# Optimization experiments

Hardware: AMD Instinct MI355X
Metric: run time of the kernel (lower is better)

Reference implementation:

```python
import jax, jax.numpy as jnp
import numpy as np

N_NODES = 50000
N_EDGES = 500000
D = 128  # input_dim == output_dim -> residual is identity


def _linear(x, W, b):
    return x @ W + b


def setup_inputs() -> dict:
    rng = np.random.default_rng(0)
    ei = rng.integers(0, N_NODES, size=(2, N_EDGES))
    # one-time structure cache: unique (src,dst) pairs + multiplicity counts
    pairs = np.stack([ei[0], ei[1]], axis=1)
    uniq, counts = np.unique(pairs, axis=0, return_counts=True)

    key = jax.random.key(0)
    ks = jax.random.split(key, 16)
    s = 0.02
    inp = {
        "x": jax.random.normal(ks[0], (N_NODES, D), jnp.float32),
        "src": jnp.asarray(uniq[:, 0], jnp.int32),
        "dst": jnp.asarray(uniq[:, 1], jnp.int32),
        "counts": jnp.asarray(counts, jnp.float32),
        # lin_src_to_dst / lin_dst_to_src (stored as [in, out])
        "W_sd": jax.random.normal(ks[1], (D, D), jnp.float32) * s,
        "b_sd": jnp.zeros((D,), jnp.float32),
        "W_ds": jax.random.normal(ks[2], (D, D), jnp.float32) * s,
        "b_ds": jnp.zeros((D,), jnp.float32),
        # lcs_mlp: Linear(2D, D) -> ReLU -> Linear(D, 1)
        "W_l1": jax.random.normal(ks[3], (2 * D, D), jnp.float32) * s,
        "b_l1": jnp.zeros((D,), jnp.float32),
        "W_l2": jax.random.normal(ks[4], (D, 1), jnp.float32) * s,
        "b_l2": jnp.zeros((1,), jnp.float32),
        # gate_mlp: Linear(2D, D) -> ReLU -> Linear(D, 1)
        "W_g1": jax.random.normal(ks[5], (2 * D, D), jnp.float32) * s,
        "b_g1": jnp.zeros((D,), jnp.float32),
        "W_g2": jax.random.normal(ks[6], (D, 1), jnp.float32) * s,
        "b_g2": jnp.zeros((1,), jnp.float32),
    }
    return inp


def reference(x, src, dst, counts, W_sd, b_sd, W_ds, b_ds,
              W_l1, b_l1, W_l2, b_l2, W_g1, b_g1, W_g2, b_g2):
    num_nodes = x.shape[0]
    x_src = x[src]                      # [E, D] gather
    x_dst = x[dst]                      # [E, D] gather

    # LCS score per unique edge (computed under no_grad in torch -> stop_gradient)
    lcs_in = jnp.concatenate([x_src, x_dst], axis=-1)           # [E, 2D]
    h = jax.nn.relu(_linear(lcs_in, W_l1, b_l1))
    lcs = jax.nn.sigmoid(_linear(h, W_l2, b_l2))                # [E, 1]
    lcs = jax.lax.stop_gradient(lcs)

    cnt = counts[:, None]                                       # [E, 1]
    msg_in = _linear(x_src, W_sd, b_sd) * lcs * cnt             # [E, D]
    msg_out = _linear(x_dst, W_ds, b_ds) * lcs * cnt            # [E, D]

    h_in = jax.ops.segment_sum(msg_in, dst, num_segments=num_nodes)
    h_out = jax.ops.segment_sum(msg_out, src, num_segments=num_nodes)

    in_deg = jnp.clip(jax.ops.segment_sum(counts, dst, num_segments=num_nodes), 1.0)
    out_deg = jnp.clip(jax.ops.segment_sum(counts, src, num_segments=num_nodes), 1.0)
    h_in = h_in / in_deg[:, None]
    h_out = h_out / out_deg[:, None]

    gate_in = jnp.concatenate([h_in, h_out], axis=-1)           # [N, 2D]
    g = jax.nn.relu(_linear(gate_in, W_g1, b_g1))
    gate = jax.nn.sigmoid(_linear(g, W_g2, b_g2))               # [N, 1]

    fused = gate * h_in + (1.0 - gate) * h_out
    return fused + x  # residual is Identity (input_dim == output_dim)
```

## Files before the change

kernel.cpp:

```cpp
#include <hip/hip_runtime.h>
#include <math.h>

typedef unsigned int uint;
typedef unsigned long long ull;

#define THREADS 256
#define NC 96

typedef __attribute__((ext_vector_type(8))) short bf16x8;
typedef __attribute__((ext_vector_type(4))) float f32x4;

__device__ __forceinline__ float blo(uint u) { return __uint_as_float(u << 16); }
__device__ __forceinline__ float bhi(uint u) { return __uint_as_float(u & 0xffff0000u); }
__device__ __forceinline__ uint  bf16r(float x) {
    uint u = __float_as_uint(x);
    return (u + 0x7fffu + ((u >> 16) & 1u)) >> 16;
}
__device__ __forceinline__ uint packbf(float lo, float hi) {
    return bf16r(lo) | (bf16r(hi) << 16);
}

__global__ __launch_bounds__(THREADS)
void transpose_w(const float* __restrict__ W_sd, const float* __restrict__ W_ds,
                 const float* __restrict__ W_l1, const float* __restrict__ W_g1,
                 ushort* __restrict__ Wt, ushort* __restrict__ Wtg1)
{
    __shared__ float tile[32][33];
    const int y = blockIdx.y;
    const float* src;
    ushort* dst;
    int dstK, kofs;
    if (y < 4) {
        src = (y == 0) ? W_sd : (y == 1) ? W_ds : (y == 2) ? W_l1 : (W_l1 + 16384);
        dst = Wt + y * 16384; dstK = 128; kofs = 0;
    } else {
        src = W_g1 + (y - 4) * 16384;
        dst = Wtg1; dstK = 256; kofs = (y - 4) * 128;
    }
    const int tix = blockIdx.x;
    const int k0 = (tix & 3) * 32, n0 = (tix >> 2) * 32;
    const int t = threadIdx.x;

    {
        const int r = t >> 3, c8 = t & 7;
        const float4 f = *(const float4*)(src + (size_t)(k0 + r) * 128 + n0 + c8 * 4);
        tile[r][c8 * 4 + 0] = f.x; tile[r][c8 * 4 + 1] = f.y;
        tile[r][c8 * 4 + 2] = f.z; tile[r][c8 * 4 + 3] = f.w;
    }
    __syncthreads();
    {
        const int n = t >> 3, k8 = t & 7;
        const float v0 = tile[k8 * 4 + 0][n], v1 = tile[k8 * 4 + 1][n];
        const float v2 = tile[k8 * 4 + 2][n], v3 = tile[k8 * 4 + 3][n];
        uint2 o; o.x = packbf(v0, v1); o.y = packbf(v2, v3);
        *(uint2*)(dst + (size_t)(n0 + n) * dstK + kofs + k0 + k8 * 4) = o;
    }
}

__device__ __forceinline__ void mfma_tile_compute(const char* AsB, const char* BtB,
                                                  int wv, int ln, f32x4 acc[8])
{
    const int mrow = wv * 16 + (ln & 15);
    const int kgb  = (ln >> 4) * 16;
#pragma unroll
    for (int kk = 0; kk < 4; ++kk) {
        const int kbyte = kk * 64 + kgb;
        const bf16x8 a = *(const bf16x8*)(AsB + mrow * 256 + (kbyte ^ ((mrow & 7) << 4)));
#pragma unroll
        for (int tt = 0; tt < 8; ++tt) {
            const int nrow = tt * 16 + (ln & 15);
            const bf16x8 b = *(const bf16x8*)(BtB + nrow * 256 + (kbyte ^ ((nrow & 7) << 4)));
            acc[tt] = __builtin_amdgcn_mfma_f32_16x16x32_bf16(a, b, acc[tt], 0, 0, 0);
        }
    }
}

__global__ __launch_bounds__(THREADS)
void gemm_node_count(const float* __restrict__ X, int M,
                     const ushort* __restrict__ Wt,
                     const float* __restrict__ b_sd, const float* __restrict__ b_ds,
                     const float* __restrict__ b_l1,
                     ushort* __restrict__ Pb,
                     const int* __restrict__ src, const int* __restrict__ dst,
                     const float* __restrict__ counts,
                     ull* __restrict__ packed_in, int* __restrict__ off_out,
                     int E)
{
    __shared__ __align__(16) char AsB[16384];
    __shared__ __align__(16) char BtB[32768];

    const int tid = threadIdx.x;
    const int bid = blockIdx.x;

    if (bid < NC) {
        const int stride = NC * THREADS;
        for (int e = bid * THREADS + tid; e < E; e += stride) {
            const int  d = dst[e];
            const uint c = (uint)counts[e];
            atomicAdd(packed_in + d, (1ULL << 32) | (ull)c);
        }
        for (int e = bid * THREADS + tid; e < E; e += stride) {
            const int cur  = src[e];
            const int prev = (e == 0) ? -1 : src[e - 1];
            for (int v = prev + 1; v <= cur; ++v) off_out[v] = e;
            if (e == E - 1)
                for (int v = cur + 1; v <= M; ++v) off_out[v] = E;
        }
        return;
    }

    const int m0 = (bid - NC) * 64;
    const int wv = tid >> 6, ln = tid & 63;

    {
        const int r = tid >> 2, seg = tid & 3;
        int gr = m0 + r; if (gr >= M) gr = M - 1;
        const float4* xs = (const float4*)(X + (size_t)gr * 128 + seg * 32);
#pragma unroll
        for (int i = 0; i < 4; ++i) {
            const float4 f0 = xs[i * 2], f1 = xs[i * 2 + 1];
            uint4 u;
            u.x = packbf(f0.x, f0.y); u.y = packbf(f0.z, f0.w);
            u.z = packbf(f1.x, f1.y); u.w = packbf(f1.z, f1.w);
            const int kbyte = seg * 64 + i * 16;
            *(uint4*)(AsB + r * 256 + (kbyte ^ ((r & 7) << 4))) = u;
        }
    }

    for (int grp = 0; grp < 4; ++grp) {
        {
            const int rn = tid >> 1, sg = tid & 1;
            const uint4* ws = (const uint4*)(Wt + grp * 16384 + (size_t)rn * 128 + sg * 64);
#pragma unroll
            for (int i = 0; i < 8; ++i) {
                const uint4 u = ws[i];
                const int kbyte = sg * 128 + i * 16;
                *(uint4*)(BtB + rn * 256 + (kbyte ^ ((rn & 7) << 4))) = u;
            }
        }
        __syncthreads();

        f32x4 acc[8];
#pragma unroll
        for (int tt = 0; tt < 8; ++tt) acc[tt] = (f32x4){0.f, 0.f, 0.f, 0.f};
        mfma_tile_compute(AsB, BtB, wv, ln, acc);
        __syncthreads();

        const float* bias = (grp == 0) ? b_sd : (grp == 1) ? b_ds
                          : (grp == 2) ? b_l1 : nullptr;
#pragma unroll
        for (int tt = 0; tt < 8; ++tt) {
            const int n  = tt * 16 + (ln & 15);
            const float bv = bias ? bias[n] : 0.f;
#pragma unroll
            for (int r = 0; r < 4; ++r) {
                const int m = wv * 16 + ((ln >> 4) << 2) + r;
                ((ushort*)BtB)[m * 136 + n] = (ushort)bf16r(acc[tt][r] + bv);
            }
        }
        __syncthreads();
        {
            const int rr = tid >> 2, sg2 = tid & 3;
            const int gr = m0 + rr;
            if (gr < M) {
                uint4* dstp = (uint4*)Pb + (size_t)gr * 64 + grp * 16 + sg2 * 4;
#pragma unroll
                for (int i = 0; i < 4; ++i)
                    dstp[i] = *(const uint4*)(BtB + rr * 272 + (sg2 * 4 + i) * 16);
            }
        }
        __syncthreads();
    }
}

__global__ __launch_bounds__(256)
void scan_p1(const ull* __restrict__ packed_in, int* __restrict__ bsum, int M)
{
    __shared__ int s[256];
    const int t = threadIdx.x;
    const int i = blockIdx.x * 256 + t;
    s[t] = (i < M) ? (int)(packed_in[i] >> 32) : 0;
    __syncthreads();
#pragma unroll
    for (int o = 128; o; o >>= 1) {
        if (t < o) s[t] += s[t + o];
        __syncthreads();
    }
    if (t == 0) bsum[blockIdx.x] = s[0];
}

__global__ __launch_bounds__(1024)
void scan_p2(int* __restrict__ bsum, int NB)
{
    __shared__ int s[1024];
    const int t = threadIdx.x;
    const int v = (t < NB) ? bsum[t] : 0;
    s[t] = v;
    __syncthreads();
    for (int o = 1; o < 1024; o <<= 1) {
        const int u = (t >= o) ? s[t - o] : 0;
        __syncthreads();
        s[t] += u;
        __syncthreads();
    }
    if (t < NB) bsum[t] = s[t] - v;
}

__global__ __launch_bounds__(256)
void scan_p3(const ull* __restrict__ packed_in, const int* __restrict__ bsum,
             int* __restrict__ off_in, int M)
{
    __shared__ int s[256];
    const int t = threadIdx.x;
    const int i = blockIdx.x * 256 + t;
    const int v = (i < M) ? (int)(packed_in[i] >> 32) : 0;
    s[t] = v;
    __syncthreads();
    for (int o = 1; o < 256; o <<= 1) {
        const int u = (t >= o) ? s[t - o] : 0;
        __syncthreads();
        s[t] += u;
        __syncthreads();
    }
    if (i < M) off_in[i] = bsum[blockIdx.x] + s[t] - v;
}

__global__ __launch_bounds__(THREADS)
void edge_lcs_fill(const ushort* __restrict__ Pb,
                   const int* __restrict__ src, const int* __restrict__ dst,
                   const float* __restrict__ counts,
                   const float* __restrict__ W_l2, const float* __restrict__ b_l2,
                   const int* __restrict__ off_in, int* __restrict__ cur_in,
                   float* __restrict__ w_e, float2* __restrict__ uw_in, int E)
{
    const int lane = threadIdx.x & 63;
    const int wid  = threadIdx.x >> 6;
    const int g    = lane >> 4;
    const int gl   = lane & 15;
    int e = (blockIdx.x * 4 + wid) * 4 + g;
    const bool valid = (e < E);
    if (!valid) e = E - 1;

    const int   s = src[e];
    const int   d = dst[e];
    const float c = counts[e];

    const uint* rs = (const uint*)Pb + (size_t)s * 256;
    const uint* rd = (const uint*)Pb + (size_t)d * 256;

    const uint4 av = ((const uint4*)(rs + 128))[gl];
    const uint4 bv = ((const uint4*)(rd + 192))[gl];

    const float4 wa = ((const float4*)W_l2)[gl * 2];
    const float4 wb = ((const float4*)W_l2)[gl * 2 + 1];

    float part =
        fmaxf(blo(av.x) + blo(bv.x), 0.f) * wa.x + fmaxf(bhi(av.x) + bhi(bv.x), 0.f) * wa.y +
        fmaxf(blo(av.y) + blo(bv.y), 0.f) * wa.z + fmaxf(bhi(av.y) + bhi(bv.y), 0.f) * wa.w +
        fmaxf(blo(av.z) + blo(bv.z), 0.f) * wb.x + fmaxf(bhi(av.z) + bhi(bv.z), 0.f) * wb.y +
        fmaxf(blo(av.w) + blo(bv.w), 0.f) * wb.z + fmaxf(bhi(av.w) + bhi(bv.w), 0.f) * wb.w;

    part += __shfl_xor(part, 1);
    part += __shfl_xor(part, 2);
    part += __shfl_xor(part, 4);
    part += __shfl_xor(part, 8);

    if (gl == 0 && valid) {
        const float lcs = 1.f / (1.f + expf(-(part + b_l2[0])));
        const float w   = lcs * c;
        w_e[e] = w;
        const int r1 = atomicAdd(cur_in + d, 1);
        uw_in[off_in[d] + r1] = make_float2(__int_as_float(s), w);
    }
}

__global__ __launch_bounds__(THREADS)
void node_agg(ushort* __restrict__ Pb,
              const float2* __restrict__ uw_in,
              const int* __restrict__ off_in, const ull* __restrict__ packed_in,
              const int* __restrict__ off_out,
              const int* __restrict__ dst, const float* __restrict__ w_e,
              const float* __restrict__ counts, int M)
{
    const int lane = threadIdx.x & 63;
    const int wid  = threadIdx.x >> 6;
    const int task = blockIdx.x * 4 + wid;
    if (task >= 2 * M) return;
    const int v   = task >> 1;
    const int dir = task & 1;

    const int g  = lane >> 4;
    const int gl = lane & 15;

    float a0 = 0.f, a1 = 0.f, a2 = 0.f, a3 = 0.f;
    float a4 = 0.f, a5 = 0.f, a6 = 0.f, a7 = 0.f;
    float dg = 0.f;

    if (dir == 0) {
        const ull pk = packed_in[v];
        const int n  = (int)(pk >> 32);
        dg = (g == 0) ? (float)(uint)(pk & 0xffffffffu) : 0.f;
        const float2* __restrict__ uw = uw_in + off_in[v];
        for (int j = g; j < n; j += 4) {
            const float2 p = uw[j];
            const int    u = __float_as_int(p.x);
            const float  w = p.y;
            const uint4 pv = ((const uint4*)((const uint*)Pb + (size_t)u * 256))[gl];
            a0 = fmaf(blo(pv.x), w, a0); a1 = fmaf(bhi(pv.x), w, a1);
            a2 = fmaf(blo(pv.y), w, a2); a3 = fmaf(bhi(pv.y), w, a3);
            a4 = fmaf(blo(pv.z), w, a4); a5 = fmaf(bhi(pv.z), w, a5);
            a6 = fmaf(blo(pv.w), w, a6); a7 = fmaf(bhi(pv.w), w, a7);
        }
    } else {
        const int base = off_out[v];
        const int end  = off_out[v + 1];
        for (int j = base + g; j < end; j += 4) {
            const int    u = dst[j];
            const float  w = w_e[j];
            dg += counts[j];
            const uint4 pv = ((const uint4*)((const uint*)Pb + (size_t)u * 256 + 64))[gl];
            a0 = fmaf(blo(pv.x), w, a0); a1 = fmaf(bhi(pv.x), w, a1);
            a2 = fmaf(blo(pv.y), w, a2); a3 = fmaf(bhi(pv.y), w, a3);
            a4 = fmaf(blo(pv.z), w, a4); a5 = fmaf(bhi(pv.z), w, a5);
            a6 = fmaf(blo(pv.w), w, a6); a7 = fmaf(bhi(pv.w), w, a7);
        }
    }

#define RED2(a) a += __shfl_xor(a, 16); a += __shfl_xor(a, 32);
    RED2(a0) RED2(a1) RED2(a2) RED2(a3) RED2(a4) RED2(a5) RED2(a6) RED2(a7) RED2(dg)
#undef RED2

    if (g == 0) {
        const float r = 1.f / fmaxf(dg, 1.f);
        uint4 o;
        o.x = packbf(a0 * r, a1 * r);
        o.y = packbf(a2 * r, a3 * r);
        o.z = packbf(a4 * r, a5 * r);
        o.w = packbf(a6 * r, a7 * r);
        ((uint4*)((uint*)Pb + (size_t)v * 256 + (dir ? 192 : 128)))[gl] = o;
    }
}

__global__ __launch_bounds__(THREADS)
void gemm_gate(ushort* __restrict__ Pb, int M,
               const ushort* __restrict__ Wtg1, const float* __restrict__ b_g1)
{
    __shared__ __align__(16) char AsB[16384];
    __shared__ __align__(16) char BtB[32768];

    const int tid = threadIdx.x;
    const int m0  = blockIdx.x * 64;
    const int wv = tid >> 6, ln = tid & 63;

    f32x4 acc[8];
#pragma unroll
    for (int tt = 0; tt < 8; ++tt) acc[tt] = (f32x4){0.f, 0.f, 0.f, 0.f};

    for (int h = 0; h < 2; ++h) {
        if (h) __syncthreads();
        {
            const int r = tid >> 2, seg = tid & 3;
            int gr = m0 + r; if (gr >= M) gr = M - 1;
            const uint4* ps = (const uint4*)Pb + (size_t)gr * 64 + 32 + h * 16 + seg * 4;
#pragma unroll
            for (int i = 0; i < 4; ++i) {
                const uint4 u = ps[i];
                const int kbyte = seg * 64 + i * 16;
                *(uint4*)(AsB + r * 256 + (kbyte ^ ((r & 7) << 4))) = u;
            }
        }
        {
            const int rn = tid >> 1, sg = tid & 1;
            const uint4* ws = (const uint4*)Wtg1 + (size_t)rn * 32 + h * 16 + sg * 8;
#pragma unroll
            for (int i = 0; i < 8; ++i) {
                const uint4 u = ws[i];
                const int kbyte = sg * 128 + i * 16;
                *(uint4*)(BtB + rn * 256 + (kbyte ^ ((rn & 7) << 4))) = u;
            }
        }
        __syncthreads();
        mfma_tile_compute(AsB, BtB, wv, ln, acc);
    }

    __syncthreads();
#pragma unroll
    for (int tt = 0; tt < 8; ++tt) {
        const int n = tt * 16 + (ln & 15);
        const float bv = b_g1[n];
#pragma unroll
        for (int r = 0; r < 4; ++r) {
            const int m = wv * 16 + ((ln >> 4) << 2) + r;
            ((ushort*)BtB)[m * 136 + n] = (ushort)bf16r(fmaxf(acc[tt][r] + bv, 0.f));
        }
    }
    __syncthreads();
    {
        const int rr = tid >> 2, sg2 = tid & 3;
        const int gr = m0 + rr;
        if (gr < M) {
            uint4* dstp = (uint4*)Pb + (size_t)gr * 64 + sg2 * 4;
#pragma unroll
            for (int i = 0; i < 4; ++i)
                dstp[i] = *(const uint4*)(BtB + rr * 272 + (sg2 * 4 + i) * 16);
        }
    }
}

__global__ __launch_bounds__(THREADS)
void finalize(const ushort* __restrict__ Pb,
              const float* __restrict__ W_g2, const float* __restrict__ b_g2,
              const float* __restrict__ x, float* __restrict__ out, int M)
{
    const int lane = threadIdx.x & 63;
    const int wid  = threadIdx.x >> 6;
    const int v    = blockIdx.x * 4 + wid;
    if (v >= M) return;

    const uint* row = (const uint*)Pb + (size_t)v * 256;

    const uint  gv = row[lane];
    const float2 w2 = *(const float2*)(W_g2 + 2 * lane);
    float part = blo(gv) * w2.x + bhi(gv) * w2.y;
#pragma unroll
    for (int off = 32; off; off >>= 1) part += __shfl_xor(part, off);
    const float gate = 1.f / (1.f + expf(-(part + b_g2[0])));

    const uint hiv = row[128 + lane];
    const uint hov = row[192 + lane];
    const float2 xv = *(const float2*)(x + (size_t)v * 128 + 2 * lane);

    float2 o;
    o.x = gate * blo(hiv) + (1.f - gate) * blo(hov) + xv.x;
    o.y = gate * bhi(hiv) + (1.f - gate) * bhi(hov) + xv.y;
    *(float2*)(out + (size_t)v * 128 + 2 * lane) = o;
}

extern "C" void kernel_launch(void* const* d_in, const int* in_sizes, int n_in,
                              void* d_out, int out_size, void* d_ws, size_t ws_size,
                              hipStream_t stream)
{
    const float* x     = (const float*)d_in[0];
    const int*   src   = (const int*)  d_in[1];
    const int*   dst   = (const int*)  d_in[2];
    const float* cnts  = (const float*)d_in[3];
    const float* W_sd  = (const float*)d_in[4];
    const float* b_sd  = (const float*)d_in[5];
    const float* W_ds  = (const float*)d_in[6];
    const float* b_ds  = (const float*)d_in[7];
    const float* W_l1  = (const float*)d_in[8];
    const float* b_l1  = (const float*)d_in[9];
    const float* W_l2  = (const float*)d_in[10];
    const float* b_l2  = (const float*)d_in[11];
    const float* W_g1  = (const float*)d_in[12];
    const float* b_g1  = (const float*)d_in[13];
    const float* W_g2  = (const float*)d_in[14];
    const float* b_g2  = (const float*)d_in[15];

    const int M = in_sizes[0] / 128;
    const int E = in_sizes[1];

    ushort* Pb        = (ushort*)d_ws;
    ushort* Wt        = Pb + (size_t)M * 512;
    ushort* Wtg1      = Wt + 4 * 16384;
    ull*    packed_in = (ull*)(Wtg1 + 32768);
    int*    cur_in    = (int*)(packed_in + M);
    float2* uw_in     = (float2*)(cur_in + M);
    int*    off_in    = (int*)(uw_in + E);
    int*    off_out   = off_in + M;
    float*  w_e       = (float*)(off_out + M + 1);
    int*    bsum      = (int*)(w_e + E);

    hipMemsetAsync(packed_in, 0, 12 * (size_t)M, stream);

    transpose_w<<<dim3(16, 6), THREADS, 0, stream>>>(W_sd, W_ds, W_l1, W_g1, Wt, Wtg1);

    const int gx = (M + 63) / 64;
    gemm_node_count<<<NC + gx, THREADS, 0, stream>>>(
        x, M, Wt, b_sd, b_ds, b_l1, Pb, src, dst, cnts, packed_in, off_out, E);

    const int NB = (M + 255) / 256;
    scan_p1<<<NB, 256, 0, stream>>>(packed_in, bsum, M);
    scan_p2<<<1, 1024, 0, stream>>>(bsum, NB);
    scan_p3<<<NB, 256, 0, stream>>>(packed_in, bsum, off_in, M);

    edge_lcs_fill<<<(E + 15) / 16, THREADS, 0, stream>>>(
        Pb, src, dst, cnts, W_l2, b_l2, off_in, cur_in, w_e, uw_in, E);

    node_agg<<<(2 * M + 3) / 4, THREADS, 0, stream>>>(
        Pb, uw_in, off_in, packed_in, off_out, dst, w_e, cnts, M);

    gemm_gate<<<gx, THREADS, 0, stream>>>(Pb, M, Wtg1, b_g1);

    finalize<<<(M + 3) / 4, THREADS, 0, stream>>>(Pb, W_g2, b_g2, x, (float*)d_out, M);
}
```

Before: 191.0 us.

## Fuse LCS edge scoring into out-aggregation and fold gate MLP into finalize

Edge LCS scoring now runs per source node inside the out-direction aggregation, so the destination row is gathered once for both the score and the message. This removes the w_e array and a separate edge pass. h_out goes to a separate buffer so the in-aggregation can run afterwards without a race. The gate GEMM kernel now also computes the gate dot product and writes the final output from LDS, dropping the finalize kernel and a round trip through global memory for the hidden activations. Packed bf16 stores via lane shuffles replace 16-bit LDS stores. The risks are load imbalance from per-node loops over skewed out-degrees and the cost of the extra kernel boundary before the in-aggregation.

```diff
diff --git a/kernel.cpp b/kernel.cpp
--- a/kernel.cpp
+++ b/kernel.cpp
@@ -155,7 +155,10 @@
 #pragma unroll
             for (int r = 0; r < 4; ++r) {
                 const int m = wv * 16 + ((ln >> 4) << 2) + r;
-                ((ushort*)BtB)[m * 136 + n] = (ushort)bf16r(acc[tt][r] + bv);
+                const float val = acc[tt][r] + bv;
+                const float pr  = __shfl_xor(val, 1);
+                if ((ln & 1) == 0)
+                    ((uint*)BtB)[m * 68 + (n >> 1)] = packbf(val, pr);
             }
         }
         __syncthreads();
@@ -226,103 +229,61 @@
 }
 
 __global__ __launch_bounds__(THREADS)
-void edge_lcs_fill(const ushort* __restrict__ Pb,
-                   const int* __restrict__ src, const int* __restrict__ dst,
-                   const float* __restrict__ counts,
-                   const float* __restrict__ W_l2, const float* __restrict__ b_l2,
-                   const int* __restrict__ off_in, int* __restrict__ cur_in,
-                   float* __restrict__ w_e, float2* __restrict__ uw_in, int E)
+void edge_out(const ushort* __restrict__ Pb, ushort* __restrict__ Hout,
+              const int* __restrict__ dst, const float* __restrict__ counts,
+              const float* __restrict__ W_l2, const float* __restrict__ b_l2,
+              const int* __restrict__ off_out,
+              const int* __restrict__ off_in, int* __restrict__ cur_in,
+              float2* __restrict__ uw_in, int M)
 {
     const int lane = threadIdx.x & 63;
     const int wid  = threadIdx.x >> 6;
-    const int g    = lane >> 4;
-    const int gl   = lane & 15;
-    int e = (blockIdx.x * 4 + wid) * 4 + g;
-    const bool valid = (e < E);
-    if (!valid) e = E - 1;
-
-    const int   s = src[e];
-    const int   d = dst[e];
-    const float c = counts[e];
-
-    const uint* rs = (const uint*)Pb + (size_t)s * 256;
-    const uint* rd = (const uint*)Pb + (size_t)d * 256;
-
+    const int v    = blockIdx.x * 4 + wid;
+    if (v >= M) return;
+    const int g  = lane >> 4;
+    const int gl = lane & 15;
+
+    const uint* rs = (const uint*)Pb + (size_t)v * 256;
     const uint4 av = ((const uint4*)(rs + 128))[gl];
-    const uint4 bv = ((const uint4*)(rd + 192))[gl];
-
     const float4 wa = ((const float4*)W_l2)[gl * 2];
     const float4 wb = ((const float4*)W_l2)[gl * 2 + 1];
-
-    float part =
-        fmaxf(blo(av.x) + blo(bv.x), 0.f) * wa.x + fmaxf(bhi(av.x) + bhi(bv.x), 0.f) * wa.y +
-        fmaxf(blo(av.y) + blo(bv.y), 0.f) * wa.z + fmaxf(bhi(av.y) + bhi(bv.y), 0.f) * wa.w +
-        fmaxf(blo(av.z) + blo(bv.z), 0.f) * wb.x + fmaxf(bhi(av.z) + bhi(bv.z), 0.f) * wb.y +
-        fmaxf(blo(av.w) + blo(bv.w), 0.f) * wb.z + fmaxf(bhi(av.w) + bhi(bv.w), 0.f) * wb.w;
-
-    part += __shfl_xor(part, 1);
-    part += __shfl_xor(part, 2);
-    part += __shfl_xor(part, 4);
-    part += __shfl_xor(part, 8);
-
-    if (gl == 0 && valid) {
-        const float lcs = 1.f / (1.f + expf(-(part + b_l2[0])));
-        const float w   = lcs * c;
-        w_e[e] = w;
-        const int r1 = atomicAdd(cur_in + d, 1);
-        uw_in[off_in[d] + r1] = make_float2(__int_as_float(s), w);
-    }
-}
-
-__global__ __launch_bounds__(THREADS)
-void node_agg(ushort* __restrict__ Pb,
-              const float2* __restrict__ uw_in,
-              const int* __restrict__ off_in, const ull* __restrict__ packed_in,
-              const int* __restrict__ off_out,
-              const int* __restrict__ dst, const float* __restrict__ w_e,
-              const float* __restrict__ counts, int M)
-{
-    const int lane = threadIdx.x & 63;
-    const int wid  = threadIdx.x >> 6;
-    const int task = blockIdx.x * 4 + wid;
-    if (task >= 2 * M) return;
-    const int v   = task >> 1;
-    const int dir = task & 1;
-
-    const int g  = lane >> 4;
-    const int gl = lane & 15;
+    const float bl2 = b_l2[0];
+
+    const int base = off_out[v];
+    const int end  = off_out[v + 1];
 
     float a0 = 0.f, a1 = 0.f, a2 = 0.f, a3 = 0.f;
     float a4 = 0.f, a5 = 0.f, a6 = 0.f, a7 = 0.f;
     float dg = 0.f;
 
-    if (dir == 0) {
-        const ull pk = packed_in[v];
-        const int n  = (int)(pk >> 32);
-        dg = (g == 0) ? (float)(uint)(pk & 0xffffffffu) : 0.f;
-        const float2* __restrict__ uw = uw_in + off_in[v];
-        for (int j = g; j < n; j += 4) {
-            const float2 p = uw[j];
-            const int    u = __float_as_int(p.x);
-            const float  w = p.y;
-            const uint4 pv = ((const uint4*)((const uint*)Pb + (size_t)u * 256))[gl];
-            a0 = fmaf(blo(pv.x), w, a0); a1 = fmaf(bhi(pv.x), w, a1);
-            a2 = fmaf(blo(pv.y), w, a2); a3 = fmaf(bhi(pv.y), w, a3);
-            a4 = fmaf(blo(pv.z), w, a4); a5 = fmaf(bhi(pv.z), w, a5);
-            a6 = fmaf(blo(pv.w), w, a6); a7 = fmaf(bhi(pv.w), w, a7);
-        }
-    } else {
-        const int base = off_out[v];
-        const int end  = off_out[v + 1];
-        for (int j = base + g; j < end; j += 4) {
-            const int    u = dst[j];
-            const float  w = w_e[j];
-            dg += counts[j];
-            const uint4 pv = ((const uint4*)((const uint*)Pb + (size_t)u * 256 + 64))[gl];
-            a0 = fmaf(blo(pv.x), w, a0); a1 = fmaf(bhi(pv.x), w, a1);
-            a2 = fmaf(blo(pv.y), w, a2); a3 = fmaf(bhi(pv.y), w, a3);
-            a4 = fmaf(blo(pv.z), w, a4); a5 = fmaf(bhi(pv.z), w, a5);
-            a6 = fmaf(blo(pv.w), w, a6); a7 = fmaf(bhi(pv.w), w, a7);
+    for (int j = base + g; j < end; j += 4) {
+        const int   d = dst[j];
+        const float c = counts[j];
+        const uint* rd = (const uint*)Pb + (size_t)d * 256;
+        const uint4 bv = ((const uint4*)(rd + 192))[gl];
+        const uint4 pv = ((const uint4*)(rd + 64))[gl];
+
+        float part =
+            fmaxf(blo(av.x) + blo(bv.x), 0.f) * wa.x + fmaxf(bhi(av.x) + bhi(bv.x), 0.f) * wa.y +
+            fmaxf(blo(av.y) + blo(bv.y), 0.f) * wa.z + fmaxf(bhi(av.y) + bhi(bv.y), 0.f) * wa.w +
+            fmaxf(blo(av.z) + blo(bv.z), 0.f) * wb.x + fmaxf(bhi(av.z) + bhi(bv.z), 0.f) * wb.y +
+            fmaxf(blo(av.w) + blo(bv.w), 0.f) * wb.z + fmaxf(bhi(av.w) + bhi(bv.w), 0.f) * wb.w;
+        part += __shfl_xor(part, 1);
+        part += __shfl_xor(part, 2);
+        part += __shfl_xor(part, 4);
+        part += __shfl_xor(part, 8);
+
+        const float w = (1.f / (1.f + expf(-(part + bl2)))) * c;
+
+        a0 = fmaf(blo(pv.x), w, a0); a1 = fmaf(bhi(pv.x), w, a1);
+        a2 = fmaf(blo(pv.y), w, a2); a3 = fmaf(bhi(pv.y), w, a3);
+        a4 = fmaf(blo(pv.z), w, a4); a5 = fmaf(bhi(pv.z), w, a5);
+        a6 = fmaf(blo(pv.w), w, a6); a7 = fmaf(bhi(pv.w), w, a7);
+        dg += c;
+
+        if (gl == 0) {
+            const int r1 = atomicAdd(cur_in + d, 1);
+            uw_in[off_in[d] + r1] = make_float2(__int_as_float(v), w);
         }
     }
 
@@ -337,13 +298,61 @@
         o.y = packbf(a2 * r, a3 * r);
         o.z = packbf(a4 * r, a5 * r);
         o.w = packbf(a6 * r, a7 * r);
-        ((uint4*)((uint*)Pb + (size_t)v * 256 + (dir ? 192 : 128)))[gl] = o;
+        ((uint4*)((uint*)Hout + (size_t)v * 64))[gl] = o;
     }
 }
 
 __global__ __launch_bounds__(THREADS)
-void gemm_gate(ushort* __restrict__ Pb, int M,
-               const ushort* __restrict__ Wtg1, const float* __restrict__ b_g1)
+void agg_in(ushort* __restrict__ Pb,
+            const float2* __restrict__ uw_in,
+            const int* __restrict__ off_in, const ull* __restrict__ packed_in,
+            int M)
+{
+    const int lane = threadIdx.x & 63;
+    const int wid  = threadIdx.x >> 6;
+    const int v    = blockIdx.x * 4 + wid;
+    if (v >= M) return;
+    const int g  = lane >> 4;
+    const int gl = lane & 15;
+
+    const ull pk = packed_in[v];
+    const int n  = (int)(pk >> 32);
+    const float dg = (float)(uint)(pk & 0xffffffffu);
+    const float2* __restrict__ uw = uw_in + off_in[v];
+
+    float a0 = 0.f, a1 = 0.f, a2 = 0.f, a3 = 0.f;
+    float a4 = 0.f, a5 = 0.f, a6 = 0.f, a7 = 0.f;
+    for (int j = g; j < n; j += 4) {
+        const float2 p = uw[j];
+        const int    u = __float_as_int(p.x);
+        const float  w = p.y;
+        const uint4 pv = ((const uint4*)((const uint*)Pb + (size_t)u * 256))[gl];
+        a0 = fmaf(blo(pv.x), w, a0); a1 = fmaf(bhi(pv.x), w, a1);
+        a2 = fmaf(blo(pv.y), w, a2); a3 = fmaf(bhi(pv.y), w, a3);
+        a4 = fmaf(blo(pv.z), w, a4); a5 = fmaf(bhi(pv.z), w, a5);
+        a6 = fmaf(blo(pv.w), w, a6); a7 = fmaf(bhi(pv.w), w, a7);
+    }
+#define RED2(a) a += __shfl_xor(a, 16); a += __shfl_xor(a, 32);
+    RED2(a0) RED2(a1) RED2(a2) RED2(a3) RED2(a4) RED2(a5) RED2(a6) RED2(a7)
+#undef RED2
+
+    if (g == 0) {
+        const float r = 1.f / fmaxf(dg, 1.f);
+        uint4 o;
+        o.x = packbf(a0 * r, a1 * r);
+        o.y = packbf(a2 * r, a3 * r);
+        o.z = packbf(a4 * r, a5 * r);
+        o.w = packbf(a6 * r, a7 * r);
+        ((uint4*)((uint*)Pb + (size_t)v * 256 + 128))[gl] = o;
+    }
+}
+
+__global__ __launch_bounds__(THREADS)
+void gate_final(const ushort* __restrict__ Pb, const ushort* __restrict__ Hout,
+                int M,
+                const ushort* __restrict__ Wtg1, const float* __restrict__ b_g1,
+                const float* __restrict__ W_g2, const float* __restrict__ b_g2,
+                const float* __restrict__ x, float* __restrict__ out)
 {
     __shared__ __align__(16) char AsB[16384];
     __shared__ __align__(16) char BtB[32768];
@@ -361,7 +370,9 @@
         {
             const int r = tid >> 2, seg = tid & 3;
             int gr = m0 + r; if (gr >= M) gr = M - 1;
-            const uint4* ps = (const uint4*)Pb + (size_t)gr * 64 + 32 + h * 16 + seg * 4;
+            const uint4* ps = (h == 0)
+                ? ((const uint4*)Pb + (size_t)gr * 64 + 32 + seg * 4)
+                : ((const uint4*)Hout + (size_t)gr * 16 + seg * 4);
 #pragma unroll
             for (int i = 0; i < 4; ++i) {
                 const uint4 u = ps[i];
@@ -391,49 +402,35 @@
 #pragma unroll
         for (int r = 0; r < 4; ++r) {
             const int m = wv * 16 + ((ln >> 4) << 2) + r;
-            ((ushort*)BtB)[m * 136 + n] = (ushort)bf16r(fmaxf(acc[tt][r] + bv, 0.f));
-        }
-    }
-    __syncthreads();
-    {
-        const int rr = tid >> 2, sg2 = tid & 3;
-        const int gr = m0 + rr;
+            const float val = fmaxf(acc[tt][r] + bv, 0.f);
+            const float pr  = __shfl_xor(val, 1);
+            if ((ln & 1) == 0)
+                ((uint*)BtB)[m * 68 + (n >> 1)] = packbf(val, pr);
+        }
+    }
+    __syncthreads();
+
+    const float bg2 = b_g2[0];
+    const float2 w2 = ((const float2*)W_g2)[ln];
+#pragma unroll 4
+    for (int r = 0; r < 16; ++r) {
+        const int row = wv * 16 + r;
+        const int gr  = m0 + row;
+        const uint gv = ((const uint*)BtB)[row * 68 + ln];
+        float part = blo(gv) * w2.x + bhi(gv) * w2.y;
+#pragma unroll
+        for (int off = 32; off; off >>= 1) part += __shfl_xor(part, off);
+        const float gate = 1.f / (1.f + expf(-(part + bg2)));
         if (gr < M) {
-            uint4* dstp = (uint4*)Pb + (size_t)gr * 64 + sg2 * 4;
-#pragma unroll
-            for (int i = 0; i < 4; ++i)
-                dstp[i] = *(const uint4*)(BtB + rr * 272 + (sg2 * 4 + i) * 16);
-        }
-    }
-}
-
-__global__ __launch_bounds__(THREADS)
-void finalize(const ushort* __restrict__ Pb,
-              const float* __restrict__ W_g2, const float* __restrict__ b_g2,
-              const float* __restrict__ x, float* __restrict__ out, int M)
-{
-    const int lane = threadIdx.x & 63;
-    const int wid  = threadIdx.x >> 6;
-    const int v    = blockIdx.x * 4 + wid;
-    if (v >= M) return;
-
-    const uint* row = (const uint*)Pb + (size_t)v * 256;
-
-    const uint  gv = row[lane];
-    const float2 w2 = *(const float2*)(W_g2 + 2 * lane);
-    float part = blo(gv) * w2.x + bhi(gv) * w2.y;
-#pragma unroll
-    for (int off = 32; off; off >>= 1) part += __shfl_xor(part, off);
-    const float gate = 1.f / (1.f + expf(-(part + b_g2[0])));
-
-    const uint hiv = row[128 + lane];
-    const uint hov = row[192 + lane];
-    const float2 xv = *(const float2*)(x + (size_t)v * 128 + 2 * lane);
-
-    float2 o;
-    o.x = gate * blo(hiv) + (1.f - gate) * blo(hov) + xv.x;
-    o.y = gate * bhi(hiv) + (1.f - gate) * bhi(hov) + xv.y;
-    *(float2*)(out + (size_t)v * 128 + 2 * lane) = o;
+            const uint hin = ((const uint*)Pb)[(size_t)gr * 256 + 128 + ln];
+            const uint hov = ((const uint*)Hout)[(size_t)gr * 64 + ln];
+            const float2 xv = ((const float2*)x)[(size_t)gr * 64 + ln];
+            float2 o;
+            o.x = gate * blo(hin) + (1.f - gate) * blo(hov) + xv.x;
+            o.y = gate * bhi(hin) + (1.f - gate) * bhi(hov) + xv.y;
+            ((float2*)out)[(size_t)gr * 64 + ln] = o;
+        }
+    }
 }
 
 extern "C" void kernel_launch(void* const* d_in, const int* in_sizes, int n_in,
@@ -463,13 +460,13 @@
     ushort* Pb        = (ushort*)d_ws;
     ushort* Wt        = Pb + (size_t)M * 512;
     ushort* Wtg1      = Wt + 4 * 16384;
-    ull*    packed_in = (ull*)(Wtg1 + 32768);
+    ushort* Hout      = Wtg1 + 32768;
+    ull*    packed_in = (ull*)(Hout + (size_t)M * 128);
     int*    cur_in    = (int*)(packed_in + M);
     float2* uw_in     = (float2*)(cur_in + M);
     int*    off_in    = (int*)(uw_in + E);
     int*    off_out   = off_in + M;
-    float*  w_e       = (float*)(off_out + M + 1);
-    int*    bsum      = (int*)(w_e + E);
+    int*    bsum      = off_out + M + 1;
 
     hipMemsetAsync(packed_in, 0, 12 * (size_t)M, stream);
 
@@ -484,13 +481,11 @@
     scan_p2<<<1, 1024, 0, stream>>>(bsum, NB);
     scan_p3<<<NB, 256, 0, stream>>>(packed_in, bsum, off_in, M);
 
-    edge_lcs_fill<<<(E + 15) / 16, THREADS, 0, stream>>>(
-        Pb, src, dst, cnts, W_l2, b_l2, off_in, cur_in, w_e, uw_in, E);
-
-    node_agg<<<(2 * M + 3) / 4, THREADS, 0, stream>>>(
-        Pb, uw_in, off_in, packed_in, off_out, dst, w_e, cnts, M);
-
-    gemm_gate<<<gx, THREADS, 0, stream>>>(Pb, M, Wtg1, b_g1);
-
-    finalize<<<(M + 3) / 4, THREADS, 0, stream>>>(Pb, W_g2, b_g2, x, (float*)d_out, M);
-}
+    edge_out<<<(M + 3) / 4, THREADS, 0, stream>>>(
+        Pb, Hout, dst, cnts, W_l2, b_l2, off_out, off_in, cur_in, uw_in, M);
+
+    agg_in<<<(M + 3) / 4, THREADS, 0, stream>>>(Pb, uw_in, off_in, packed_in, M);
+
+    gate_final<<<gx, THREADS, 0, stream>>>(Pb, Hout, M, Wtg1, b_g1, W_g2, b_g2,
+                                           x, (float*)d_out);
+}
```

Measured after the change: 200.2 us. 4.8% more time.
